# Optimization experiments

Measured on AMD Instinct MI355X. Metric: run time of the kernel, lower is better.

## Reference

```python
import jax, jax.numpy as jnp
import numpy as np

B, L, C = 2, 8192, 256
K, NLEV = 17, 4
HALF = K // 2


def setup_inputs() -> dict:
    key = jax.random.key(0)
    ks = jax.random.split(key, 10)
    s = 0.02
    return {
        "x": jax.random.normal(ks[0], (B, L, C), jnp.float32),
        "stem_w": jax.random.normal(ks[1], (C, C, 2), jnp.float32) * s,   # Conv1d (out,in,k)
        "stem_b": jax.random.normal(ks[2], (C,), jnp.float32) * s,
        "qkv_w": jax.random.normal(ks[3], (3 * C, C), jnp.float32) * s,
        "width_w": jax.random.normal(ks[4], (1, C), jnp.float32) * s,
        "width_b": jax.random.normal(ks[5], (1,), jnp.float32) * s,
        "out_w": jax.random.normal(ks[6], (C, C), jnp.float32) * s,
        "query": jax.random.normal(ks[7], (NLEV * C,), jnp.float32) * s,
        "film_w": jax.random.normal(ks[8], (2 * C, NLEV * C), jnp.float32) * s,
        "film_b": jax.random.normal(ks[9], (2 * C,), jnp.float32) * s,
    }


def _local_attn(h, qkv_w, width_w, width_b, out_w):
    # h: (b, l, c); 1D local windowed attention with learned sigmoid distance mask
    b, l, c = h.shape
    rel_dist = jnp.abs(jnp.arange(K, dtype=h.dtype) - HALF)  # (K,)
    max_dist = float(HALF)
    scale = c ** -0.5
    qkv = h @ qkv_w.T
    q, k, v = jnp.split(qkv, 3, axis=-1)
    width = jax.nn.sigmoid(h @ width_w.T + width_b) * max_dist + 0.5  # (b,l,1)
    k_pad = jnp.pad(k, ((0, 0), (HALF, HALF), (0, 0)))
    v_pad = jnp.pad(v, ((0, 0), (HALF, HALF), (0, 0)))
    idx = jnp.arange(l)[:, None] + jnp.arange(K)[None, :]  # (l,K) indices into padded seq
    k_win = k_pad[:, idx]  # (b,l,K,c)
    v_win = v_pad[:, idx]  # (b,l,K,c)
    scores = jnp.einsum('blc,blwc->blw', q, k_win) * scale
    soft_mask = jax.nn.sigmoid((width - rel_dist) * 5.0)  # (b,l,K)
    scores = scores - (1.0 - soft_mask) * 10000.0
    attn = jax.nn.softmax(scores, axis=-1)
    o = jnp.einsum('blw,blwc->blc', attn, v_win)
    return (o + v) @ out_w.T


def _forward(x, stem_w, stem_b, qkv_w, width_w, width_b, out_w, query, film_w, film_b):
    b, l, c = x.shape
    # stem conv: Conv1d(C, C, kernel=2, padding=1), then narrow to first l positions
    h = jnp.transpose(x, (0, 2, 1))  # (B,C,L)
    h = jax.lax.conv_general_dilated(h, stem_w, (1,), [(1, 1)],
                                     dimension_numbers=('NCH', 'OIH', 'NCH'))
    h = h[:, :, :l] + stem_b[None, :, None]
    h = jnp.transpose(h, (0, 2, 1))  # (B,L,C)
    levels = []
    for i in range(NLEV):
        h = _local_attn(h, qkv_w, width_w, width_b, out_w)
        levels.append(h)
        if i < NLEV - 1:  # avg_pool(kernel=2, stride=2)
            bl = h.shape[1]
            h = h.reshape(b, bl // 2, 2, c).mean(axis=2)
    # nearest upsample each coarser level back to L (factors are exact powers of 2)
    ups = [levels[0]]
    for lvl in levels[1:]:
        ups.append(jnp.repeat(lvl, l // lvl.shape[1], axis=1))
    concat = jnp.concatenate(ups, axis=-1)  # (B,L,NLEV*C)
    gattn = jax.nn.softmax(concat @ query, axis=-1)  # (B,L)
    global_ctx = jnp.einsum('bl,bld->bd', gattn, concat)  # (B,NLEV*C)
    film = global_ctx @ film_w.T + film_b  # (B,2C)
    scale_f, bias_f = jnp.split(film, 2, axis=-1)
    return levels[0] * (1.0 + scale_f[:, None, :]) + bias_f[:, None, :]


def reference(x, stem_w, stem_b, qkv_w, width_w, width_b, out_w, query, film_w, film_b):
    return _forward(x, stem_w, stem_b, qkv_w, width_w, width_b, out_w, query, film_w, film_b)
```

## Files before the change

kernel.cpp:

```cpp
#include <hip/hip_runtime.h>
#include <math.h>

#define L_SEQ 8192
#define B_SZ  2
#define CH    256
#define NLEV  4

typedef __attribute__((ext_vector_type(8))) short bf16x8;
typedef __attribute__((ext_vector_type(4))) float f32x4;

static __device__ __forceinline__ float sigmoidf_(float x) {
    return 1.0f / (1.0f + expf(-x));
}

static __device__ __forceinline__ float bf2f_(unsigned short u) {
    union { unsigned int ui; float f; } x;
    x.ui = ((unsigned int)u) << 16;
    return x.f;
}
static __device__ __forceinline__ unsigned short f2b_(float f) {
    union { float f; unsigned int u; } x;
    x.f = f;
    unsigned int lsb = (x.u >> 16) & 1u;
    unsigned int r = x.u + 0x7fffu + lsb;
    return (unsigned short)(r >> 16);
}
static __device__ __forceinline__ float4 ldb4_(const unsigned short* p) {
    ushort4 u = *(const ushort4*)p;
    return make_float4(bf2f_(u.x), bf2f_(u.y), bf2f_(u.z), bf2f_(u.w));
}

#define NPREP_BLOCKS 17409
__global__ __launch_bounds__(256) void prep_kernel(
    const float* __restrict__ x, const float* __restrict__ qkv_w,
    const float* __restrict__ out_w, const float* __restrict__ stem_w,
    unsigned short* __restrict__ x16g, unsigned short* __restrict__ qw16,
    unsigned short* __restrict__ sw16)
{
    __shared__ float owr[256];
    if (blockIdx.x >= NPREP_BLOCKS) {
        const int c = blockIdx.x - NPREP_BLOCKS, j = threadIdx.x;
        owr[j] = out_w[(size_t)c * 256 + j];
        __syncthreads();
        float acc = 0.0f;
        #pragma unroll 8
        for (int k = 0; k < 256; ++k)
            acc += owr[k] * qkv_w[(size_t)(512 + k) * 256 + j];
        qw16[(size_t)(512 + c) * 256 + j] = f2b_(acc);
        return;
    }
    int i = blockIdx.x * 256 + threadIdx.x;
    if (i < 256) { x16g[i] = 0; return; }
    i -= 256;
    if (i < 4194304) { x16g[256 + i] = f2b_(x[i]); return; }
    i -= 4194304;
    if (i < 131072) { qw16[i] = f2b_(qkv_w[i]); return; }
    i -= 131072;
    {
        int k = i & 511, nn = i >> 9;
        float v = (k < 256) ? stem_w[(size_t)nn * 512 + k * 2]
                            : stem_w[(size_t)nn * 512 + (k - 256) * 2 + 1];
        sw16[i] = f2b_(v);
    }
}

template<int STEM>
__global__ __launch_bounds__(1024, 1) void level_fused_kernel(
    const unsigned short* __restrict__ h16in, const unsigned short* __restrict__ x16g,
    const unsigned short* __restrict__ sw, const float* __restrict__ sbias,
    const unsigned short* __restrict__ qw,
    const float* __restrict__ ww, const float* __restrict__ wbp,
    unsigned short* __restrict__ l16o, unsigned short* __restrict__ dsB, int l)
{
    __shared__ __align__(16) char smem[127232];
    unsigned short* hs = (unsigned short*)smem;
    unsigned short* xs = (unsigned short*)(smem + 40960);
    unsigned short* qs = (unsigned short*)(smem + 40960);
    unsigned short* ks = (unsigned short*)(smem + 73728);
    unsigned short* vt = (unsigned short*)(smem + 40960);
    unsigned short* pb = (unsigned short*)(smem + 114688);
    float* sp1 = (float*)(smem + 118784);
    float* ws1 = (float*)(smem + 126976);

    const int tid  = threadIdx.x;
    const int wave = tid >> 6;
    const int lane = tid & 63;
    const int rt8  = wave & 3;
    const int half = (wave >> 2) & 1;
    const int q    = lane >> 4;
    const int n    = lane & 15;
    const int ct   = wave;

    int bid = blockIdx.x;
    const int cpx = gridDim.x >> 3;
    bid = (bid & 7) * cpx + (bid >> 3);

    const int bps = l >> 6;
    const int b  = bid / bps;
    const int t0 = (bid % bps) << 6;
    const size_t seqbase = (size_t)b * l;

    if constexpr (STEM) {
        #pragma unroll
        for (int i = 0; i < 3; ++i) {
            const int task = i * 1024 + tid;
            if (task < 2592) {
                const int r = task >> 5, ch = task & 31;
                const int gx = t0 - 9 + r;
                const unsigned short* src = (gx >= 0 && gx < l)
                    ? x16g + ((size_t)(seqbase + gx) + 1) * 256 + ((ch ^ (r & 7)) << 3)
                    : x16g;
                __builtin_amdgcn_global_load_lds(
                    (const __attribute__((address_space(1))) void*)src,
                    (__attribute__((address_space(3))) void*)
                        (xs + (size_t)(i * 1024 + (tid & ~63)) * 8),
                    16, 0, 0);
            }
        }
        __syncthreads();

        f32x4 accA[5] = {};
        #pragma unroll
        for (int pass = 0; pass < 2; ++pass) {
            bf16x8 wA[8];
            const unsigned short* wa_ = sw + (size_t)(ct * 16 + n) * 512 + pass * 256 + q * 8;
            #pragma unroll
            for (int j = 0; j < 8; ++j) wA[j] = *(const bf16x8*)(wa_ + j * 32);
            #pragma unroll
            for (int rtile = 0; rtile < 5; ++rtile) {
                const int xr = rtile * 16 + n + pass;
                const int xswz = (xr & 7) << 4;
                bf16x8 af[8];
                #pragma unroll
                for (int j = 0; j < 8; ++j)
                    af[j] = *(const bf16x8*)((const char*)xs +
                             ((xr * 512 + (j * 32 + q * 8) * 2) ^ xswz));
                #pragma unroll
                for (int j = 0; j < 8; ++j)
                    accA[rtile] = __builtin_amdgcn_mfma_f32_16x16x32_bf16(
                        af[j], wA[j], accA[rtile], 0, 0, 0);
            }
        }
        const float bA = sbias[ct * 16 + n];
        #pragma unroll
        for (int rtile = 0; rtile < 5; ++rtile)
            #pragma unroll
            for (int idx = 0; idx < 4; ++idx) {
                const int row = rtile * 16 + q * 4 + idx;
                const int growh = t0 - 8 + row;
                const int rswz = (row & 7) << 4;
                const bool ok = (growh >= 0 && growh < l);
                *(unsigned short*)((char*)hs +
                    ((row * 512 + (ct * 16 + n) * 2) ^ rswz)) =
                        ok ? f2b_(accA[rtile][idx] + bA) : (unsigned short)0;
            }
        __syncthreads();
    } else {
        #pragma unroll
        for (int i = 0; i < 3; ++i) {
            const int task = i * 1024 + tid;
            if (task < 2560) {
                const int r = task >> 5, ch = task & 31;
                const int grow = t0 - 8 + r;
                const unsigned short* src = (grow >= 0 && grow < l)
                    ? h16in + (seqbase + grow) * 256 + ((ch ^ (r & 7)) << 3)
                    : x16g;
                __builtin_amdgcn_global_load_lds(
                    (const __attribute__((address_space(1))) void*)src,
                    (__attribute__((address_space(3))) void*)
                        (hs + (size_t)(i * 1024 + (tid & ~63)) * 8),
                    16, 0, 0);
            }
        }
        __syncthreads();
    }

    {
        bf16x8 bwa[8];
        const unsigned short* wa_ = qw + (size_t)(ct * 16 + n) * 256 + q * 8;
        #pragma unroll
        for (int j = 0; j < 8; ++j) bwa[j] = *(const bf16x8*)(wa_ + j * 32);
        #pragma unroll
        for (int rtq = 0; rtq < 4; ++rtq) {
            const int hr = 8 + rtq * 16 + n;
            const int hswz = (hr & 7) << 4;
            bf16x8 af[8];
            #pragma unroll
            for (int j = 0; j < 8; ++j)
                af[j] = *(const bf16x8*)((const char*)hs +
                         ((hr * 512 + (j * 32 + q * 8) * 2) ^ hswz));
            f32x4 aA = {};
            #pragma unroll
            for (int j = 0; j < 8; ++j)
                aA = __builtin_amdgcn_mfma_f32_16x16x32_bf16(af[j], bwa[j], aA, 0, 0, 0);
            #pragma unroll
            for (int idx = 0; idx < 4; ++idx) {
                const int row = rtq * 16 + q * 4 + idx;
                const int rswz = (row & 7) << 4;
                *(unsigned short*)((char*)qs +
                    ((row * 512 + (ct * 16 + n) * 2) ^ rswz)) = f2b_(aA[idx]);
            }
        }
    }
    {
        bf16x8 bwa[8];
        const unsigned short* wa_ = qw + (size_t)(256 + ct * 16 + n) * 256 + q * 8;
        #pragma unroll
        for (int j = 0; j < 8; ++j) bwa[j] = *(const bf16x8*)(wa_ + j * 32);
        #pragma unroll
        for (int rtk = 0; rtk < 5; ++rtk) {
            const int hr = rtk * 16 + n;
            const int hswz = (hr & 7) << 4;
            bf16x8 af[8];
            #pragma unroll
            for (int j = 0; j < 8; ++j)
                af[j] = *(const bf16x8*)((const char*)hs +
                         ((hr * 512 + (j * 32 + q * 8) * 2) ^ hswz));
            f32x4 aA = {};
            #pragma unroll
            for (int j = 0; j < 8; ++j)
                aA = __builtin_amdgcn_mfma_f32_16x16x32_bf16(af[j], bwa[j], aA, 0, 0, 0);
            #pragma unroll
            for (int idx = 0; idx < 4; ++idx) {
                const int row = rtk * 16 + q * 4 + idx;
                const int rswz = (row & 7) << 4;
                *(unsigned short*)((char*)ks +
                    ((row * 512 + (ct * 16 + n) * 2) ^ rswz)) = f2b_(aA[idx]);
            }
        }
    }
    __syncthreads();

    float wdot = 0.0f;
    f32x4 accS[2] = {};
    if (wave < 8) {
        const int kc0 = half * 128;
        {
            const int hr = 8 + rt8 * 16 + n;
            const int hswz = (hr & 7) << 4;
            #pragma unroll
            for (int jj = 0; jj < 4; ++jj) {
                bf16x8 hv = *(const bf16x8*)((const char*)hs +
                            ((hr * 512 + (kc0 + q * 32 + jj * 8) * 2) ^ hswz));
                float4 wa = *((const float4*)(ww + kc0 + q * 32 + jj * 8));
                float4 wc = *((const float4*)(ww + kc0 + q * 32 + jj * 8 + 4));
                wdot += bf2f_((unsigned short)hv[0]) * wa.x
                      + bf2f_((unsigned short)hv[1]) * wa.y
                      + bf2f_((unsigned short)hv[2]) * wa.z
                      + bf2f_((unsigned short)hv[3]) * wa.w
                      + bf2f_((unsigned short)hv[4]) * wc.x
                      + bf2f_((unsigned short)hv[5]) * wc.y
                      + bf2f_((unsigned short)hv[6]) * wc.z
                      + bf2f_((unsigned short)hv[7]) * wc.w;
            }
        }
        wdot += __shfl_xor(wdot, 16, 64);
        wdot += __shfl_xor(wdot, 32, 64);
        if (half == 1 && q == 0) ws1[rt8 * 16 + n] = wdot;

        {
            const int qrow = rt8 * 16 + n;
            const int qswz = (qrow & 7) << 4;
            bf16x8 qf[4];
            #pragma unroll
            for (int j = 0; j < 4; ++j)
                qf[j] = *(const bf16x8*)((const char*)qs +
                         ((qrow * 512 + (kc0 + q * 8 + j * 32) * 2) ^ qswz));
            #pragma unroll
            for (int h = 0; h < 2; ++h) {
                const int rk = rt8 * 16 + h * 16 + n;
                const int kswz = (rk & 7) << 4;
                #pragma unroll
                for (int j = 0; j < 4; ++j) {
                    bf16x8 kb = *(const bf16x8*)((const char*)ks +
                                ((rk * 512 + (kc0 + q * 8 + j * 32) * 2) ^ kswz));
                    accS[h] = __builtin_amdgcn_mfma_f32_16x16x32_bf16(
                        qf[j], kb, accS[h], 0, 0, 0);
                }
            }
        }
        if (half == 1) {
            *(f32x4*)(sp1 + ((rt8 * 2 + 0) * 64 + lane) * 4) = accS[0];
            *(f32x4*)(sp1 + ((rt8 * 2 + 1) * 64 + lane) * 4) = accS[1];
        }
    }
    __syncthreads();

    if (wave < 4) {
        accS[0] += *(const f32x4*)(sp1 + ((rt8 * 2 + 0) * 64 + lane) * 4);
        accS[1] += *(const f32x4*)(sp1 + ((rt8 * 2 + 1) * 64 + lane) * 4);
        const float w_n = sigmoidf_(wdot + ws1[rt8 * 16 + n] + wbp[0]) * 8.0f + 0.5f;

        float wd[4];
        #pragma unroll
        for (int r = 0; r < 4; ++r) wd[r] = __shfl(w_n, q * 4 + r, 64);

        float s[2][4];
        #pragma unroll
        for (int h = 0; h < 2; ++h)
            #pragma unroll
            for (int r = 0; r < 4; ++r) {
                int ii = q * 4 + r;
                int c  = h * 16 + n;
                int w  = c - ii;
                float dist = fabsf((float)w - 8.0f);
                float sm = sigmoidf_((wd[r] - dist) * 5.0f);
                float v = accS[h][r] * 0.0625f - (1.0f - sm) * 10000.0f;
                s[h][r] = (w >= 0 && w <= 16) ? v : -3.0e38f;
            }

        float mx[4], sum[4];
        #pragma unroll
        for (int r = 0; r < 4; ++r) mx[r] = fmaxf(s[0][r], s[1][r]);
        #pragma unroll
        for (int m = 1; m < 16; m <<= 1)
            #pragma unroll
            for (int r = 0; r < 4; ++r) mx[r] = fmaxf(mx[r], __shfl_xor(mx[r], m, 64));
        float e[2][4];
        #pragma unroll
        for (int h = 0; h < 2; ++h)
            #pragma unroll
            for (int r = 0; r < 4; ++r) e[h][r] = expf(s[h][r] - mx[r]);
        #pragma unroll
        for (int r = 0; r < 4; ++r) sum[r] = e[0][r] + e[1][r];
        #pragma unroll
        for (int m = 1; m < 16; m <<= 1)
            #pragma unroll
            for (int r = 0; r < 4; ++r) sum[r] += __shfl_xor(sum[r], m, 64);

        #pragma unroll
        for (int h = 0; h < 2; ++h)
            #pragma unroll
            for (int r = 0; r < 4; ++r) {
                int ii = q * 4 + r, c = h * 16 + n;
                float p = e[h][r] / sum[r];
                if (c == ii + 8) p += 1.0f;
                pb[rt8 * 512 + ii * 32 + c] = f2b_(p);
            }
    }
    __syncthreads();

    {
        bf16x8 bwa[8];
        const unsigned short* wa_ = qw + (size_t)(512 + ct * 16 + n) * 256 + q * 8;
        #pragma unroll
        for (int j = 0; j < 8; ++j) bwa[j] = *(const bf16x8*)(wa_ + j * 32);
        #pragma unroll
        for (int rtv = 0; rtv < 5; ++rtv) {
            const int hr = rtv * 16 + n;
            const int hswz = (hr & 7) << 4;
            bf16x8 af[8];
            #pragma unroll
            for (int j = 0; j < 8; ++j)
                af[j] = *(const bf16x8*)((const char*)hs +
                         ((hr * 512 + (j * 32 + q * 8) * 2) ^ hswz));
            f32x4 aA = {};
            #pragma unroll
            for (int j = 0; j < 8; ++j)
                aA = __builtin_amdgcn_mfma_f32_16x16x32_bf16(af[j], bwa[j], aA, 0, 0, 0);
            ushort4 pA;
            pA.x = f2b_(aA[0]); pA.y = f2b_(aA[1]); pA.z = f2b_(aA[2]); pA.w = f2b_(aA[3]);
            const int rb = rtv * 16 + q * 4;
            *(ushort4*)(vt + (size_t)(ct * 16 + n) * 88 + rb) = pA;
        }
    }
    __syncthreads();

    {
        const int rtp = wave & 3;
        const int ctq = wave >> 2;
        bf16x8 pf = *(const bf16x8*)(pb + rtp * 512 + n * 32 + q * 8);
        const int rl = q * 4;
        const int row0 = t0 + rtp * 16;
        const size_t gbase = seqbase + row0;
        #pragma unroll
        for (int c = 0; c < 4; ++c) {
            const int ctp = ctq * 4 + c;
            bf16x8 vf = *(const bf16x8*)(vt + (ctp * 16 + n) * 88 + rtp * 16 + q * 8);
            f32x4 z = {};
            f32x4 o = __builtin_amdgcn_mfma_f32_16x16x32_bf16(pf, vf, z, 0, 0, 0);
            const int col = ctp * 16 + n;
            float v0 = o[0], v1 = o[1], v2 = o[2], v3 = o[3];
            size_t r0 = (gbase + rl) * CH + col;
            l16o[r0]          = f2b_(v0);
            l16o[r0 + CH]     = f2b_(v1);
            l16o[r0 + 2 * CH] = f2b_(v2);
            l16o[r0 + 3 * CH] = f2b_(v3);
            if (dsB) {
                size_t d0 = ((gbase + rl) >> 1) * CH + col;
                dsB[d0]      = f2b_(0.5f * (v0 + v1));
                dsB[d0 + CH] = f2b_(0.5f * (v2 + v3));
            }
        }
    }
}

__global__ __launch_bounds__(1024) void tail_ctx_kernel(
    const unsigned short* __restrict__ l0, const unsigned short* __restrict__ l1,
    const unsigned short* __restrict__ l2, const unsigned short* __restrict__ l3,
    const float* __restrict__ query, float* __restrict__ partials,
    float* __restrict__ denomP)
{
    __shared__ float eS[128];
    const int tid = threadIdx.x;
    const int chunk = blockIdx.x, b = blockIdx.y;
    const int t0 = chunk * 128;
    const unsigned short* levp[4] = {l0, l1, l2, l3};

    const int w = tid >> 6, lane = tid & 63;
    const int lev = lane >> 4, c0 = (lane & 15) * 16;
    const unsigned short* lpbase = levp[lev] + (size_t)b * (L_SEQ >> lev) * CH;
    const float* qp = query + lev * CH + c0;
    float4 q0 = *(const float4*)(qp);
    float4 q1 = *(const float4*)(qp + 4);
    float4 q2 = *(const float4*)(qp + 8);
    float4 q3 = *(const float4*)(qp + 12);
    #pragma unroll
    for (int j = 0; j < 8; ++j) {
        int t = t0 + w * 8 + j;
        const unsigned short* p = lpbase + (size_t)(t >> lev) * CH + c0;
        float4 h0 = ldb4_(p), h1 = ldb4_(p + 4), h2 = ldb4_(p + 8), h3 = ldb4_(p + 12);
        float part = h0.x * q0.x + h0.y * q0.y + h0.z * q0.z + h0.w * q0.w
                   + h1.x * q1.x + h1.y * q1.y + h1.z * q1.z + h1.w * q1.w
                   + h2.x * q2.x + h2.y * q2.y + h2.z * q2.z + h2.w * q2.w
                   + h3.x * q3.x + h3.y * q3.y + h3.z * q3.z + h3.w * q3.w;
        #pragma unroll
        for (int m = 1; m < 64; m <<= 1) part += __shfl_xor(part, m, 64);
        if (lane == 0) eS[w * 8 + j] = expf(part);
    }
    __syncthreads();

    if (tid == 0) {
        float ds = 0.0f;
        #pragma unroll 8
        for (int i = 0; i < 128; ++i) ds += eS[i];
        denomP[b * 64 + chunk] = ds;
    }

    const int dlev = tid >> 8, c = tid & 255;
    const unsigned short* lp = levp[dlev] + (size_t)b * (L_SEQ >> dlev) * CH;
    float acc = 0.0f;
    #pragma unroll 4
    for (int t = t0; t < t0 + 128; ++t)
        acc += eS[t - t0] * bf2f_(lp[(size_t)(t >> dlev) * CH + c]);
    partials[(size_t)(b * 64 + chunk) * 1024 + tid] = acc;
}

__global__ __launch_bounds__(256) void film_kernel(
    const float* __restrict__ partials, const float* __restrict__ denomP,
    const float* __restrict__ fw, const float* __restrict__ fb,
    float* __restrict__ film)
{
    __shared__ float ctxS[2048];
    const int tid = threadIdx.x;

    float den[2];
    #pragma unroll
    for (int b = 0; b < 2; ++b) {
        float d = 0.0f;
        #pragma unroll
        for (int c = 0; c < 64; ++c) d += denomP[b * 64 + c];
        den[b] = d;
    }
    #pragma unroll
    for (int v = 0; v < 8; ++v) {
        const int idx = v * 256 + tid;
        const int b = idx >> 10, d = idx & 1023;
        float acc = 0.0f;
        #pragma unroll
        for (int c = 0; c < 64; ++c)
            acc += partials[(size_t)(b * 64 + c) * 1024 + d];
        ctxS[idx] = acc / den[b];
    }
    __syncthreads();

    const int lane = tid & 63;
    const int j = blockIdx.x * 4 + (tid >> 6);
    float acc0 = 0.0f, acc1 = 0.0f;
    #pragma unroll
    for (int r = 0; r < 4; ++r) {
        float4 w4 = *((const float4*)(fw + (size_t)j * 1024 + r * 256) + lane);
        float4 c0 = *((const float4*)(ctxS + r * 256) + lane);
        float4 c1 = *((const float4*)(ctxS + 1024 + r * 256) + lane);
        acc0 += w4.x * c0.x + w4.y * c0.y + w4.z * c0.z + w4.w * c0.w;
        acc1 += w4.x * c1.x + w4.y * c1.y + w4.z * c1.z + w4.w * c1.w;
    }
    #pragma unroll
    for (int m = 1; m < 64; m <<= 1) {
        acc0 += __shfl_xor(acc0, m, 64);
        acc1 += __shfl_xor(acc1, m, 64);
    }
    if (lane == 0) {
        float b = fb[j];
        film[j] = acc0 + b;
        film[512 + j] = acc1 + b;
    }
}

__global__ void final_kernel(const unsigned short* __restrict__ lev0,
                             const float* __restrict__ film,
                             float* __restrict__ out)
{
    size_t n4 = ((size_t)blockIdx.x * 256 + threadIdx.x) * 4;
    int c = (int)(n4 & (CH - 1));
    int b = (int)(n4 >> 21);
    float4 h = ldb4_(lev0 + n4);
    const float* fs = film + b * 512;
    float4 o;
    o.x = h.x * (1.0f + fs[c + 0]) + fs[256 + c + 0];
    o.y = h.y * (1.0f + fs[c + 1]) + fs[256 + c + 1];
    o.z = h.z * (1.0f + fs[c + 2]) + fs[256 + c + 2];
    o.w = h.w * (1.0f + fs[c + 3]) + fs[256 + c + 3];
    *(float4*)(out + n4) = o;
}

extern "C" void kernel_launch(void* const* d_in, const int* in_sizes, int n_in,
                              void* d_out, int out_size, void* d_ws, size_t ws_size,
                              hipStream_t stream) {
    const float* x       = (const float*)d_in[0];
    const float* stem_w  = (const float*)d_in[1];
    const float* stem_b  = (const float*)d_in[2];
    const float* qkv_w   = (const float*)d_in[3];
    const float* width_w = (const float*)d_in[4];
    const float* width_b = (const float*)d_in[5];
    const float* out_w   = (const float*)d_in[6];
    const float* query   = (const float*)d_in[7];
    const float* film_w  = (const float*)d_in[8];
    const float* film_b  = (const float*)d_in[9];
    float* out = (float*)d_out;
    float* ws  = (float*)d_ws;

    float* partials = ws;
    float* denomP   = partials + 131072;
    float* ctx      = denomP + 128;
    float* film     = ctx + 2048;
    unsigned short* x16g  = (unsigned short*)(film + 1024);
    unsigned short* h16_0 = x16g + 4194560;
    unsigned short* h16_1 = h16_0 + 4194304;
    unsigned short* h16_2 = h16_1 + 2097152;
    unsigned short* h16_3 = h16_2 + 1048576;
    unsigned short* qkv16 = h16_3 + 524288;
    unsigned short* ov16  = qkv16 + 12582912;
    unsigned short* l16_0 = ov16 + 4194304;
    unsigned short* l16_1 = l16_0 + 4194304;
    unsigned short* l16_2 = l16_1 + 2097152;
    unsigned short* l16_3 = l16_2 + 1048576;
    unsigned short* qw16  = l16_3 + 524288;
    unsigned short* ow16  = qw16 + 196608;
    unsigned short* sw16  = ow16 + 65536;
    unsigned short* h16[4]  = {h16_0, h16_1, h16_2, h16_3};
    unsigned short* l16[4]  = {l16_0, l16_1, l16_2, l16_3};
    (void)qkv16; (void)ov16; (void)ow16; (void)ctx;

    prep_kernel<<<NPREP_BLOCKS + 256, 256, 0, stream>>>(
        x, qkv_w, out_w, stem_w, x16g, qw16, sw16);

    for (int i = 0; i < NLEV; ++i) {
        const int l = L_SEQ >> i;
        const int M = B_SZ * l;
        if (i == 0)
            level_fused_kernel<1><<<M / 64, 1024, 0, stream>>>(
                h16[0], x16g, sw16, stem_b, qw16, width_w, width_b,
                l16[0], h16_1, l);
        else
            level_fused_kernel<0><<<M / 64, 1024, 0, stream>>>(
                h16[i], x16g, sw16, stem_b, qw16, width_w, width_b,
                l16[i], (i < NLEV - 1) ? h16[i + 1] : nullptr, l);
    }

    tail_ctx_kernel<<<dim3(64, B_SZ), 1024, 0, stream>>>(
        l16_0, l16_1, l16_2, l16_3, query, partials, denomP);
    film_kernel<<<128, 256, 0, stream>>>(partials, denomP, film_w, film_b, film);
    final_kernel<<<(B_SZ * L_SEQ * CH) / 1024, 256, 0, stream>>>(l16_0, film, out);
}
```

Measured before the change: 218.7 us.

## Fuse all levels and tail stages into one cooperative persistent kernel

Replaces the four per-level launches plus the tail, film and final kernels with a single cooperative kernel of 256 blocks that runs each stage in turn, separated by grid-wide syncs. The aim is to remove kernel-launch gaps and tail-drain overhead between the small, dependent stages. In exchange, later levels leave most blocks idle, and each grid.sync has its own cost. Cooperative launch also needs all 256 blocks of 1024 threads with about 124KB of LDS to be resident at once, one per CU.

```diff
diff --git a/kernel.cpp b/kernel.cpp
--- a/kernel.cpp
+++ b/kernel.cpp
@@ -1,10 +1,13 @@
 #include <hip/hip_runtime.h>
+#include <hip/hip_cooperative_groups.h>
 #include <math.h>
 
 #define L_SEQ 8192
 #define B_SZ  2
 #define CH    256
 #define NLEV  4
+
+namespace cg = cooperative_groups;
 
 typedef __attribute__((ext_vector_type(8))) short bf16x8;
 typedef __attribute__((ext_vector_type(4))) float f32x4;
@@ -65,14 +68,14 @@
 }
 
 template<int STEM>
-__global__ __launch_bounds__(1024, 1) void level_fused_kernel(
+static __device__ void do_level(
+    char* smem, int lbid, int nwg,
     const unsigned short* __restrict__ h16in, const unsigned short* __restrict__ x16g,
     const unsigned short* __restrict__ sw, const float* __restrict__ sbias,
     const unsigned short* __restrict__ qw,
     const float* __restrict__ ww, const float* __restrict__ wbp,
     unsigned short* __restrict__ l16o, unsigned short* __restrict__ dsB, int l)
 {
-    __shared__ __align__(16) char smem[127232];
     unsigned short* hs = (unsigned short*)smem;
     unsigned short* xs = (unsigned short*)(smem + 40960);
     unsigned short* qs = (unsigned short*)(smem + 40960);
@@ -91,8 +94,8 @@
     const int n    = lane & 15;
     const int ct   = wave;
 
-    int bid = blockIdx.x;
-    const int cpx = gridDim.x >> 3;
+    int bid = lbid;
+    const int cpx = nwg >> 3;
     bid = (bid & 7) * cpx + (bid >> 3);
 
     const int bps = l >> 6;
@@ -395,123 +398,153 @@
     }
 }
 
-__global__ __launch_bounds__(1024) void tail_ctx_kernel(
-    const unsigned short* __restrict__ l0, const unsigned short* __restrict__ l1,
-    const unsigned short* __restrict__ l2, const unsigned short* __restrict__ l3,
-    const float* __restrict__ query, float* __restrict__ partials,
-    float* __restrict__ denomP)
+struct MegaParams {
+    const unsigned short* x16g;
+    const unsigned short* sw;
+    const float* sbias;
+    const unsigned short* qw;
+    const float* ww;
+    const float* wbp;
+    unsigned short *l0, *l1, *l2, *l3;
+    unsigned short *h1, *h2, *h3;
+    const float* query;
+    float* partials;
+    float* denomP;
+    const float* fw;
+    const float* fb;
+    float* film;
+    float* out;
+};
+
+__global__ __launch_bounds__(1024, 1) void mega_kernel(MegaParams p)
 {
-    __shared__ float eS[128];
+    __shared__ __align__(16) char smem[127232];
+    cg::grid_group grid = cg::this_grid();
+    const int blk = blockIdx.x;
     const int tid = threadIdx.x;
-    const int chunk = blockIdx.x, b = blockIdx.y;
-    const int t0 = chunk * 128;
-    const unsigned short* levp[4] = {l0, l1, l2, l3};
-
-    const int w = tid >> 6, lane = tid & 63;
-    const int lev = lane >> 4, c0 = (lane & 15) * 16;
-    const unsigned short* lpbase = levp[lev] + (size_t)b * (L_SEQ >> lev) * CH;
-    const float* qp = query + lev * CH + c0;
-    float4 q0 = *(const float4*)(qp);
-    float4 q1 = *(const float4*)(qp + 4);
-    float4 q2 = *(const float4*)(qp + 8);
-    float4 q3 = *(const float4*)(qp + 12);
+
+    do_level<1>(smem, blk, 256, nullptr, p.x16g, p.sw, p.sbias, p.qw,
+                p.ww, p.wbp, p.l0, p.h1, L_SEQ);
+    grid.sync();
+    if (blk < 128)
+        do_level<0>(smem, blk, 128, p.h1, p.x16g, p.sw, p.sbias, p.qw,
+                    p.ww, p.wbp, p.l1, p.h2, L_SEQ >> 1);
+    grid.sync();
+    if (blk < 64)
+        do_level<0>(smem, blk, 64, p.h2, p.x16g, p.sw, p.sbias, p.qw,
+                    p.ww, p.wbp, p.l2, p.h3, L_SEQ >> 2);
+    grid.sync();
+    if (blk < 32)
+        do_level<0>(smem, blk, 32, p.h3, p.x16g, p.sw, p.sbias, p.qw,
+                    p.ww, p.wbp, p.l3, nullptr, L_SEQ >> 3);
+    grid.sync();
+
+    if (blk < 128) {
+        float* eS = (float*)smem;
+        const int chunk = blk & 63, b = blk >> 6;
+        const int t0 = chunk * 128;
+        const unsigned short* levp[4] = {p.l0, p.l1, p.l2, p.l3};
+
+        const int w = tid >> 6, lane = tid & 63;
+        const int lev = lane >> 4, c0 = (lane & 15) * 16;
+        const unsigned short* lpbase = levp[lev] + (size_t)b * (L_SEQ >> lev) * CH;
+        const float* qp = p.query + lev * CH + c0;
+        float4 q0 = *(const float4*)(qp);
+        float4 q1 = *(const float4*)(qp + 4);
+        float4 q2 = *(const float4*)(qp + 8);
+        float4 q3 = *(const float4*)(qp + 12);
+        #pragma unroll
+        for (int j = 0; j < 8; ++j) {
+            int t = t0 + w * 8 + j;
+            const unsigned short* pp = lpbase + (size_t)(t >> lev) * CH + c0;
+            float4 h0 = ldb4_(pp), h1 = ldb4_(pp + 4), h2 = ldb4_(pp + 8), h3 = ldb4_(pp + 12);
+            float part = h0.x * q0.x + h0.y * q0.y + h0.z * q0.z + h0.w * q0.w
+                       + h1.x * q1.x + h1.y * q1.y + h1.z * q1.z + h1.w * q1.w
+                       + h2.x * q2.x + h2.y * q2.y + h2.z * q2.z + h2.w * q2.w
+                       + h3.x * q3.x + h3.y * q3.y + h3.z * q3.z + h3.w * q3.w;
+            #pragma unroll
+            for (int m = 1; m < 64; m <<= 1) part += __shfl_xor(part, m, 64);
+            if (lane == 0) eS[w * 8 + j] = expf(part);
+        }
+        __syncthreads();
+
+        if (tid == 0) {
+            float ds = 0.0f;
+            #pragma unroll 8
+            for (int i = 0; i < 128; ++i) ds += eS[i];
+            p.denomP[b * 64 + chunk] = ds;
+        }
+
+        const int dlev = tid >> 8, c = tid & 255;
+        const unsigned short* lp = levp[dlev] + (size_t)b * (L_SEQ >> dlev) * CH;
+        float acc = 0.0f;
+        #pragma unroll 4
+        for (int t = t0; t < t0 + 128; ++t)
+            acc += eS[t - t0] * bf2f_(lp[(size_t)(t >> dlev) * CH + c]);
+        p.partials[(size_t)(b * 64 + chunk) * 1024 + tid] = acc;
+    }
+    grid.sync();
+
+    if (blk < 32) {
+        float* ctxS = (float*)smem;
+        float den[2];
+        #pragma unroll
+        for (int b = 0; b < 2; ++b) {
+            float d = 0.0f;
+            #pragma unroll
+            for (int c = 0; c < 64; ++c) d += p.denomP[b * 64 + c];
+            den[b] = d;
+        }
+        #pragma unroll
+        for (int v = 0; v < 2; ++v) {
+            const int idx = v * 1024 + tid;
+            const int b = idx >> 10, d = idx & 1023;
+            float acc = 0.0f;
+            #pragma unroll
+            for (int c = 0; c < 64; ++c)
+                acc += p.partials[(size_t)(b * 64 + c) * 1024 + d];
+            ctxS[idx] = acc / den[b];
+        }
+        __syncthreads();
+
+        const int lane = tid & 63;
+        const int j = blk * 16 + (tid >> 6);
+        float acc0 = 0.0f, acc1 = 0.0f;
+        #pragma unroll
+        for (int r = 0; r < 4; ++r) {
+            float4 w4 = *((const float4*)(p.fw + (size_t)j * 1024 + r * 256) + lane);
+            float4 c0 = *((const float4*)(ctxS + r * 256) + lane);
+            float4 c1 = *((const float4*)(ctxS + 1024 + r * 256) + lane);
+            acc0 += w4.x * c0.x + w4.y * c0.y + w4.z * c0.z + w4.w * c0.w;
+            acc1 += w4.x * c1.x + w4.y * c1.y + w4.z * c1.z + w4.w * c1.w;
+        }
+        #pragma unroll
+        for (int m = 1; m < 64; m <<= 1) {
+            acc0 += __shfl_xor(acc0, m, 64);
+            acc1 += __shfl_xor(acc1, m, 64);
+        }
+        if (lane == 0) {
+            float b = p.fb[j];
+            p.film[j] = acc0 + b;
+            p.film[512 + j] = acc1 + b;
+        }
+    }
+    grid.sync();
+
     #pragma unroll
-    for (int j = 0; j < 8; ++j) {
-        int t = t0 + w * 8 + j;
-        const unsigned short* p = lpbase + (size_t)(t >> lev) * CH + c0;
-        float4 h0 = ldb4_(p), h1 = ldb4_(p + 4), h2 = ldb4_(p + 8), h3 = ldb4_(p + 12);
-        float part = h0.x * q0.x + h0.y * q0.y + h0.z * q0.z + h0.w * q0.w
-                   + h1.x * q1.x + h1.y * q1.y + h1.z * q1.z + h1.w * q1.w
-                   + h2.x * q2.x + h2.y * q2.y + h2.z * q2.z + h2.w * q2.w
-                   + h3.x * q3.x + h3.y * q3.y + h3.z * q3.z + h3.w * q3.w;
-        #pragma unroll
-        for (int m = 1; m < 64; m <<= 1) part += __shfl_xor(part, m, 64);
-        if (lane == 0) eS[w * 8 + j] = expf(part);
-    }
-    __syncthreads();
-
-    if (tid == 0) {
-        float ds = 0.0f;
-        #pragma unroll 8
-        for (int i = 0; i < 128; ++i) ds += eS[i];
-        denomP[b * 64 + chunk] = ds;
-    }
-
-    const int dlev = tid >> 8, c = tid & 255;
-    const unsigned short* lp = levp[dlev] + (size_t)b * (L_SEQ >> dlev) * CH;
-    float acc = 0.0f;
-    #pragma unroll 4
-    for (int t = t0; t < t0 + 128; ++t)
-        acc += eS[t - t0] * bf2f_(lp[(size_t)(t >> dlev) * CH + c]);
-    partials[(size_t)(b * 64 + chunk) * 1024 + tid] = acc;
-}
-
-__global__ __launch_bounds__(256) void film_kernel(
-    const float* __restrict__ partials, const float* __restrict__ denomP,
-    const float* __restrict__ fw, const float* __restrict__ fb,
-    float* __restrict__ film)
-{
-    __shared__ float ctxS[2048];
-    const int tid = threadIdx.x;
-
-    float den[2];
-    #pragma unroll
-    for (int b = 0; b < 2; ++b) {
-        float d = 0.0f;
-        #pragma unroll
-        for (int c = 0; c < 64; ++c) d += denomP[b * 64 + c];
-        den[b] = d;
-    }
-    #pragma unroll
-    for (int v = 0; v < 8; ++v) {
-        const int idx = v * 256 + tid;
-        const int b = idx >> 10, d = idx & 1023;
-        float acc = 0.0f;
-        #pragma unroll
-        for (int c = 0; c < 64; ++c)
-            acc += partials[(size_t)(b * 64 + c) * 1024 + d];
-        ctxS[idx] = acc / den[b];
-    }
-    __syncthreads();
-
-    const int lane = tid & 63;
-    const int j = blockIdx.x * 4 + (tid >> 6);
-    float acc0 = 0.0f, acc1 = 0.0f;
-    #pragma unroll
-    for (int r = 0; r < 4; ++r) {
-        float4 w4 = *((const float4*)(fw + (size_t)j * 1024 + r * 256) + lane);
-        float4 c0 = *((const float4*)(ctxS + r * 256) + lane);
-        float4 c1 = *((const float4*)(ctxS + 1024 + r * 256) + lane);
-        acc0 += w4.x * c0.x + w4.y * c0.y + w4.z * c0.z + w4.w * c0.w;
-        acc1 += w4.x * c1.x + w4.y * c1.y + w4.z * c1.z + w4.w * c1.w;
-    }
-    #pragma unroll
-    for (int m = 1; m < 64; m <<= 1) {
-        acc0 += __shfl_xor(acc0, m, 64);
-        acc1 += __shfl_xor(acc1, m, 64);
-    }
-    if (lane == 0) {
-        float b = fb[j];
-        film[j] = acc0 + b;
-        film[512 + j] = acc1 + b;
-    }
-}
-
-__global__ void final_kernel(const unsigned short* __restrict__ lev0,
-                             const float* __restrict__ film,
-                             float* __restrict__ out)
-{
-    size_t n4 = ((size_t)blockIdx.x * 256 + threadIdx.x) * 4;
-    int c = (int)(n4 & (CH - 1));
-    int b = (int)(n4 >> 21);
-    float4 h = ldb4_(lev0 + n4);
-    const float* fs = film + b * 512;
-    float4 o;
-    o.x = h.x * (1.0f + fs[c + 0]) + fs[256 + c + 0];
-    o.y = h.y * (1.0f + fs[c + 1]) + fs[256 + c + 1];
-    o.z = h.z * (1.0f + fs[c + 2]) + fs[256 + c + 2];
-    o.w = h.w * (1.0f + fs[c + 3]) + fs[256 + c + 3];
-    *(float4*)(out + n4) = o;
+    for (int it = 0; it < 4; ++it) {
+        size_t n4 = ((size_t)it * 262144 + (size_t)blk * 1024 + tid) * 4;
+        int c = (int)(n4 & (CH - 1));
+        int b = (int)(n4 >> 21);
+        float4 h = ldb4_(p.l0 + n4);
+        const float* fs = p.film + b * 512;
+        float4 o;
+        o.x = h.x * (1.0f + fs[c + 0]) + fs[256 + c + 0];
+        o.y = h.y * (1.0f + fs[c + 1]) + fs[256 + c + 1];
+        o.z = h.z * (1.0f + fs[c + 2]) + fs[256 + c + 2];
+        o.w = h.w * (1.0f + fs[c + 3]) + fs[256 + c + 3];
+        *(float4*)(p.out + n4) = o;
+    }
 }
 
 extern "C" void kernel_launch(void* const* d_in, const int* in_sizes, int n_in,
@@ -548,28 +581,20 @@
     unsigned short* qw16  = l16_3 + 524288;
     unsigned short* ow16  = qw16 + 196608;
     unsigned short* sw16  = ow16 + 65536;
-    unsigned short* h16[4]  = {h16_0, h16_1, h16_2, h16_3};
-    unsigned short* l16[4]  = {l16_0, l16_1, l16_2, l16_3};
-    (void)qkv16; (void)ov16; (void)ow16; (void)ctx;
+    (void)h16_0; (void)qkv16; (void)ov16; (void)ow16;
 
     prep_kernel<<<NPREP_BLOCKS + 256, 256, 0, stream>>>(
         x, qkv_w, out_w, stem_w, x16g, qw16, sw16);
 
-    for (int i = 0; i < NLEV; ++i) {
-        const int l = L_SEQ >> i;
-        const int M = B_SZ * l;
-        if (i == 0)
-            level_fused_kernel<1><<<M / 64, 1024, 0, stream>>>(
-                h16[0], x16g, sw16, stem_b, qw16, width_w, width_b,
-                l16[0], h16_1, l);
-        else
-            level_fused_kernel<0><<<M / 64, 1024, 0, stream>>>(
-                h16[i], x16g, sw16, stem_b, qw16, width_w, width_b,
-                l16[i], (i < NLEV - 1) ? h16[i + 1] : nullptr, l);
-    }
-
-    tail_ctx_kernel<<<dim3(64, B_SZ), 1024, 0, stream>>>(
-        l16_0, l16_1, l16_2, l16_3, query, partials, denomP);
-    film_kernel<<<128, 256, 0, stream>>>(partials, denomP, film_w, film_b, film);
-    final_kernel<<<(B_SZ * L_SEQ * CH) / 1024, 256, 0, stream>>>(l16_0, film, out);
-}
+    MegaParams p;
+    p.x16g = x16g; p.sw = sw16; p.sbias = stem_b; p.qw = qw16;
+    p.ww = width_w; p.wbp = width_b;
+    p.l0 = l16_0; p.l1 = l16_1; p.l2 = l16_2; p.l3 = l16_3;
+    p.h1 = h16_1; p.h2 = h16_2; p.h3 = h16_3;
+    p.query = query; p.partials = partials; p.denomP = denomP;
+    p.fw = film_w; p.fb = film_b; p.film = film; p.out = out;
+
+    void* args[] = { &p };
+    hipLaunchCooperativeKernel((const void*)mega_kernel, dim3(256), dim3(1024),
+                               args, 0, stream);
+}
```

Result: slower. 421.6 us (+92.8%).
